# Optimization experiments

Hardware: AMD Instinct MI355X
Metric: run time of the kernel (lower is better)

## Reference

```python
import jax, jax.numpy as jnp
import numpy as np

H = 8            # heads actually used for the q/k/v split (256 = 8 * 32)
D = 32           # per-head dim
SCALE = 64 ** -0.5  # original code scales by init-arg dim_head**-0.5 (=64), not the actual split dim


def setup_inputs() -> dict:
    key = jax.random.key(0)
    ks = jax.random.split(key, 7)
    b, nq, nk, dim = 4, 2048, 2048, 256
    s = 1.0 / np.sqrt(dim).astype(np.float32)
    c2 = jax.random.normal(ks[0], (b, nk, dim), jnp.float32)
    c1 = jax.random.normal(ks[1], (b, nq, dim), jnp.float32)
    # weights stored as [in, out] so y = x @ W (equivalent to torch Linear)
    Wq = jax.random.normal(ks[2], (dim, dim), jnp.float32) * s
    Wk = jax.random.normal(ks[3], (dim, dim), jnp.float32) * s
    Wv = jax.random.normal(ks[4], (dim, dim), jnp.float32) * s
    Wo = jax.random.normal(ks[5], (dim, dim), jnp.float32) * s
    bo = jax.random.normal(ks[6], (dim,), jnp.float32) * 0.01
    return {"c2": c2, "c1": c1, "Wq": Wq, "Wk": Wk, "Wv": Wv, "Wo": Wo, "bo": bo}


def reference(c2, c1, Wq, Wk, Wv, Wo, bo):
    b, nq, dim = c1.shape
    nk = c2.shape[1]
    q = (c1 @ Wq).reshape(b, nq, H, D)   # queries from c1
    k = (c2 @ Wk).reshape(b, nk, H, D)   # keys from c2
    v = (c2 @ Wv).reshape(b, nk, H, D)   # values from c2
    dots = jnp.einsum('bqhd,bkhd->bhqk', q, k) * SCALE  # [b,H,nq,nk]
    attn = jax.nn.softmax(dots, axis=-1)
    out = jnp.einsum('bhqk,bkhd->bqhd', attn, v).reshape(b, nq, dim)
    return out @ Wo + bo  # to_out projection (dropout=0.0 -> identity)
```

## Files before the change

### kernel.cpp

```cpp
#include <hip/hip_runtime.h>
#include <hip/hip_bf16.h>

typedef __bf16 bf16;
typedef __bf16 bf16x4 __attribute__((ext_vector_type(4)));
typedef __bf16 bf16x8 __attribute__((ext_vector_type(8)));
typedef float f32x4 __attribute__((ext_vector_type(4)));

#define MFMA(a, b, c) __builtin_amdgcn_mfma_f32_16x16x32_bf16(a, b, c, 0, 0, 0)

#define QSCALE (0.125f * 1.44269504088896340736f)

#define OFF_Q  262144
#define OFF_K  (OFF_Q + 2097152)
#define OFF_VT (OFF_K + 2097152)
#define OFF_P  (OFF_VT + 2097152)
#define OFF_L  (OFF_P + 4194304)

static __device__ __forceinline__ float fexp2(float x) {
    return __builtin_amdgcn_exp2f(x);
}

#define GLL16(g, l)                                                              \
    __builtin_amdgcn_global_load_lds(                                            \
        (const __attribute__((address_space(1))) void*)(g),                      \
        (__attribute__((address_space(3))) void*)(l), 16, 0, 0)

__global__ __launch_bounds__(256) void k_wt(const float* __restrict__ Wq,
                                            const float* __restrict__ Wk,
                                            const float* __restrict__ Wv,
                                            const float* __restrict__ Wo,
                                            bf16* __restrict__ wts) {
    __shared__ __align__(16) bf16 tile[64][64];
    int rb = blockIdx.x, ob = blockIdx.y, mat = blockIdx.z;
    const float* src = (mat == 0) ? Wq : (mat == 1) ? Wk : (mat == 2) ? Wv : Wo;
    int t = threadIdx.x;
    int lr = t >> 4, lc = (t & 15) * 4;
#pragma unroll
    for (int rr = 0; rr < 4; ++rr) {
        int i = rb * 64 + rr * 16 + lr;
        f32x4 a = *reinterpret_cast<const f32x4*>(src + (size_t)i * 256 + ob * 64 + lc);
        bf16x4 v;
#pragma unroll
        for (int j = 0; j < 4; ++j) v[j] = (bf16)a[j];
        *reinterpret_cast<bf16x4*>(&tile[rr * 16 + lr][lc]) = v;
    }
    __syncthreads();
    int ol = t >> 2, ib = (t & 3) * 16;
    int o = ob * 64 + ol;
    bf16x8 v0, v1;
#pragma unroll
    for (int k = 0; k < 8; ++k) {
        v0[k] = tile[ib + k][ol];
        v1[k] = tile[ib + 8 + k][ol];
    }
    bf16* dst = wts + (size_t)mat * 65536 + (size_t)o * 256 + rb * 64 + ib;
    *reinterpret_cast<bf16x8*>(dst) = v0;
    *reinterpret_cast<bf16x8*>(dst + 8) = v1;
}

__global__ __launch_bounds__(384) void k_proj(const float* __restrict__ c1,
                                              const float* __restrict__ c2,
                                              const bf16* __restrict__ wts,
                                              bf16* __restrict__ qkv) {
    __shared__ __align__(16) bf16 sA[2][4096];
    int m = blockIdx.x;
    int t = threadIdx.x;

    if (t < 256) {
        int row = t >> 4, c0t = t & 15;
        const float* ap = c1 + ((size_t)m * 16 + row) * 256 + c0t * 16;
        f32x4 a0 = *reinterpret_cast<const f32x4*>(ap);
        f32x4 a1 = *reinterpret_cast<const f32x4*>(ap + 4);
        f32x4 a2 = *reinterpret_cast<const f32x4*>(ap + 8);
        f32x4 a3 = *reinterpret_cast<const f32x4*>(ap + 12);
        bf16x8 w0, w1;
#pragma unroll
        for (int j = 0; j < 4; ++j) {
            w0[j] = (bf16)a0[j]; w0[j + 4] = (bf16)a1[j];
            w1[j] = (bf16)a2[j]; w1[j + 4] = (bf16)a3[j];
        }
        int kc = c0t >> 1, gA = (c0t & 1) * 2;
        *reinterpret_cast<bf16x8*>(&sA[0][kc * 512 + (gA * 16 + row) * 8]) = w0;
        *reinterpret_cast<bf16x8*>(&sA[0][kc * 512 + ((gA + 1) * 16 + row) * 8]) = w1;
    }
    if (t >= 128) {
        int t2 = t - 128;
        int row = t2 >> 4, c0t = t2 & 15;
        const float* ap = c2 + ((size_t)m * 16 + row) * 256 + c0t * 16;
        f32x4 a0 = *reinterpret_cast<const f32x4*>(ap);
        f32x4 a1 = *reinterpret_cast<const f32x4*>(ap + 4);
        f32x4 a2 = *reinterpret_cast<const f32x4*>(ap + 8);
        f32x4 a3 = *reinterpret_cast<const f32x4*>(ap + 12);
        bf16x8 w0, w1;
#pragma unroll
        for (int j = 0; j < 4; ++j) {
            w0[j] = (bf16)a0[j]; w0[j + 4] = (bf16)a1[j];
            w1[j] = (bf16)a2[j]; w1[j + 4] = (bf16)a3[j];
        }
        int kc = c0t >> 1, gA = (c0t & 1) * 2;
        *reinterpret_cast<bf16x8*>(&sA[1][kc * 512 + (gA * 16 + row) * 8]) = w0;
        *reinterpret_cast<bf16x8*>(&sA[1][kc * 512 + ((gA + 1) * 16 + row) * 8]) = w1;
    }
    __syncthreads();

    int u = t >> 6;
    int lane = t & 63, cc = lane & 15, g = lane >> 4;
    int mat = u >> 1, nh = u & 1;
    const bf16* wt = wts + (size_t)mat * 65536;
    const bf16* sAp = sA[mat == 0 ? 0 : 1];

    f32x4 acc[8] = {};
#pragma unroll
    for (int kc = 0; kc < 8; ++kc) {
        bf16x8 af = *reinterpret_cast<const bf16x8*>(&sAp[kc * 512 + lane * 8]);
#pragma unroll
        for (int ct = 0; ct < 8; ++ct) {
            bf16x8 bf = *reinterpret_cast<const bf16x8*>(
                wt + (size_t)(nh * 128 + ct * 16 + cc) * 256 + kc * 32 + g * 8);
            acc[ct] = (mat == 2) ? MFMA(bf, af, acc[ct])
                                 : MFMA(af, bf, acc[ct]);
        }
    }

    if (mat != 2) {
        float os = (mat == 0) ? QSCALE : 1.0f;
        bf16* dst = qkv + (size_t)mat * 2097152;
#pragma unroll
        for (int ct = 0; ct < 8; ++ct) {
            int col = nh * 128 + ct * 16 + cc;
#pragma unroll
            for (int j = 0; j < 4; ++j)
                dst[(size_t)(m * 16 + 4 * g + j) * 256 + col] = (bf16)(acc[ct][j] * os);
        }
    } else {
        bf16* vt = qkv + (size_t)2 * 2097152;
        int b = (m * 16) >> 11, n0 = (m * 16) & 2047;
#pragma unroll
        for (int ct = 0; ct < 8; ++ct) {
#pragma unroll
            for (int j = 0; j < 4; ++j)
                vt[((size_t)b * 256 + nh * 128 + ct * 16 + 4 * g + j) * 2048 + n0 + cc] =
                    (bf16)acc[ct][j];
        }
    }
}

__global__ __launch_bounds__(256, 4) void k_attn(const bf16* __restrict__ Q,
                                                 const bf16* __restrict__ K,
                                                 const bf16* __restrict__ Vt,
                                                 bf16* __restrict__ P,
                                                 float* __restrict__ Lf) {
    __shared__ __align__(16) bf16 sK[4][2048];
    __shared__ __align__(16) bf16 sV[4][2048];

    int flat = blockIdx.x;
    int xcd = flat & 7;
    int sub = flat >> 3;
    int bh = xcd * 4 + (sub & 3);
    int rest = sub >> 2;
    int xtile = rest & 15;
    int split = rest >> 4;

    int b = bh >> 3, hd = bh & 7;
    int kv0 = split << 10;
    int lane = threadIdx.x & 63;
    int w = threadIdx.x >> 6;
    int cc = lane & 15, g = lane >> 4;
    int qrow0 = xtile * 128 + w * 32;

    const bf16* Qh = Q + (size_t)(b * 2048) * 256 + hd * 32;
    const bf16* Vth = Vt + (size_t)bh * 65536;
    size_t kbase0 = (size_t)(b * 2048) * 256 + hd * 32;

    bf16x8 qf[2];
#pragma unroll
    for (int h = 0; h < 2; ++h)
        qf[h] = *reinterpret_cast<const bf16x8*>(
            Qh + (size_t)(qrow0 + h * 16 + cc) * 256 + g * 8);

    int kp0 = 8 * (cc >> 2) + (cc & 3);
    int kperm[4];
#pragma unroll
    for (int r = 0; r < 4; ++r) kperm[r] = 32 * (r >> 1) + 4 * (r & 1) + kp0;

    int krow = w * 16 + (lane >> 2);
    int kcol = (lane & 3) * 8;
    int dv = w * 8 + (lane >> 3);
    int vcol = ((lane & 7) ^ (lane >> 3)) * 8;

    float lsum[2] = {0.f, 0.f};
    f32x4 oA[2] = {}, oB[2] = {};

#define STAGE(t, buf)                                                           \
    do {                                                                        \
        int kb_ = kv0 + (t) * 64;                                               \
        const bf16* kg_ = K + kbase0 + (size_t)(kb_ + krow) * 256 + kcol;       \
        GLL16(kg_, &sK[buf][w * 512]);                                          \
        const bf16* vg_ = Vth + (size_t)dv * 2048 + kb_ + vcol;                 \
        GLL16(vg_, &sV[buf][w * 512]);                                          \
    } while (0)

    STAGE(0, 0);
    STAGE(1, 1);

    for (int kt = 0; kt < 16; ++kt) {
        int cur = kt & 3;
        if (kt + 2 < 16) STAGE(kt + 2, (kt + 2) & 3);

        asm volatile("s_waitcnt vmcnt(4)" ::: "memory");
        __builtin_amdgcn_s_barrier();
        __builtin_amdgcn_sched_barrier(0);

        bf16x8 kf[4], vf[4];
#pragma unroll
        for (int r = 0; r < 4; ++r)
            kf[r] = *reinterpret_cast<const bf16x8*>(&sK[cur][kperm[r] * 32 + g * 8]);
#pragma unroll
        for (int dt = 0; dt < 2; ++dt)
#pragma unroll
            for (int kk = 0; kk < 2; ++kk) {
                int colp = (kk * 4 + g) ^ (cc & 7);
                vf[dt * 2 + kk] = *reinterpret_cast<const bf16x8*>(
                    &sV[cur][(dt * 16 + cc) * 64 + colp * 8]);
            }

#pragma unroll
        for (int h = 0; h < 2; ++h) {
            f32x4 z = {};
            f32x4 s[4];
            __builtin_amdgcn_s_setprio(1);
#pragma unroll
            for (int r = 0; r < 4; ++r) s[r] = MFMA(kf[r], qf[h], z);
            __builtin_amdgcn_s_setprio(0);

#pragma unroll
            for (int r = 0; r < 4; ++r)
#pragma unroll
                for (int j = 0; j < 4; ++j) s[r][j] = fexp2(s[r][j]);
            float t0 = (s[0][0] + s[0][1]) + (s[0][2] + s[0][3]);
            float t1 = (s[1][0] + s[1][1]) + (s[1][2] + s[1][3]);
            float t2 = (s[2][0] + s[2][1]) + (s[2][2] + s[2][3]);
            float t3 = (s[3][0] + s[3][1]) + (s[3][2] + s[3][3]);
            lsum[h] += (t0 + t1) + (t2 + t3);

            bf16x8 pb[2];
#pragma unroll
            for (int kk = 0; kk < 2; ++kk)
#pragma unroll
                for (int e = 0; e < 8; ++e)
                    pb[kk][e] = (bf16)s[2 * kk + (e >> 2)][e & 3];

            __builtin_amdgcn_s_setprio(1);
            oA[h] = MFMA(vf[0], pb[0], oA[h]);
            oA[h] = MFMA(vf[1], pb[1], oA[h]);
            oB[h] = MFMA(vf[2], pb[0], oB[h]);
            oB[h] = MFMA(vf[3], pb[1], oB[h]);
            __builtin_amdgcn_s_setprio(0);
        }
    }
#undef STAGE

#pragma unroll
    for (int h = 0; h < 2; ++h) {
        lsum[h] += __shfl_xor(lsum[h], 16);
        lsum[h] += __shfl_xor(lsum[h], 32);

        bf16* Pp = P + (size_t)split * 2097152 +
                   ((size_t)b * 2048 + qrow0 + h * 16 + cc) * 256 + hd * 32;
        bf16x4 w0, w1;
#pragma unroll
        for (int j = 0; j < 4; ++j) {
            w0[j] = (bf16)oA[h][j];
            w1[j] = (bf16)oB[h][j];
        }
        *reinterpret_cast<bf16x4*>(Pp + 4 * g) = w0;
        *reinterpret_cast<bf16x4*>(Pp + 16 + 4 * g) = w1;
        if (g == 0)
            Lf[(size_t)split * 65536 + (size_t)bh * 2048 + qrow0 + h * 16 + cc] = lsum[h];
    }
}

__global__ __launch_bounds__(64) void k_out(const bf16* __restrict__ P,
                                            const float* __restrict__ Lf,
                                            const bf16* __restrict__ WoT,
                                            const float* __restrict__ bo,
                                            float* __restrict__ out) {
    int m = blockIdx.x, nb = blockIdx.y;
    int l = threadIdx.x;
    int cc = l & 15, g = l >> 4;
    int arow = m * 16 + cc;
    int b = arow >> 11, n = arow & 2047;

    f32x4 acc[4] = {};
#pragma unroll
    for (int kc = 0; kc < 8; ++kc) {
        float l0 = Lf[(size_t)(b * 8 + kc) * 2048 + n];
        float l1 = Lf[65536 + (size_t)(b * 8 + kc) * 2048 + n];
        float inv = 1.0f / (l0 + l1);
        bf16x8 p0 = *reinterpret_cast<const bf16x8*>(
            P + (size_t)arow * 256 + kc * 32 + g * 8);
        bf16x8 p1 = *reinterpret_cast<const bf16x8*>(
            P + 2097152 + (size_t)arow * 256 + kc * 32 + g * 8);
        bf16x8 af;
#pragma unroll
        for (int e = 0; e < 8; ++e)
            af[e] = (bf16)(((float)p0[e] + (float)p1[e]) * inv);
#pragma unroll
        for (int ct = 0; ct < 4; ++ct) {
            bf16x8 bf = *reinterpret_cast<const bf16x8*>(
                WoT + (size_t)(nb * 64 + ct * 16 + cc) * 256 + kc * 32 + g * 8);
            acc[ct] = MFMA(af, bf, acc[ct]);
        }
    }
#pragma unroll
    for (int ct = 0; ct < 4; ++ct) {
        int col = nb * 64 + ct * 16 + cc;
        float bias = bo[col];
#pragma unroll
        for (int j = 0; j < 4; ++j) {
            int row = m * 16 + 4 * g + j;
            out[(size_t)row * 256 + col] = acc[ct][j] + bias;
        }
    }
}

extern "C" void kernel_launch(void* const* d_in, const int* in_sizes, int n_in,
                              void* d_out, int out_size, void* d_ws, size_t ws_size,
                              hipStream_t stream) {
    const float* c2 = (const float*)d_in[0];
    const float* c1 = (const float*)d_in[1];
    const float* Wq = (const float*)d_in[2];
    const float* Wk = (const float*)d_in[3];
    const float* Wv = (const float*)d_in[4];
    const float* Wo = (const float*)d_in[5];
    const float* bo = (const float*)d_in[6];
    float* out = (float*)d_out;

    bf16* ws = (bf16*)d_ws;
    bf16* wts = ws;
    bf16* Q = ws + OFF_Q;
    bf16* Vt = ws + OFF_VT;
    bf16* P = ws + OFF_P;
    float* Lf = (float*)(ws + OFF_L);

    k_wt<<<dim3(4, 4, 4), 256, 0, stream>>>(Wq, Wk, Wv, Wo, wts);
    k_proj<<<dim3(512), 384, 0, stream>>>(c1, c2, wts, Q);
    k_attn<<<dim3(1024), 256, 0, stream>>>(Q, ws + OFF_K, Vt, P, Lf);
    k_out<<<dim3(512, 4), 64, 0, stream>>>(P, Lf, wts + 3 * 65536, bo, out);
}
```

Baseline: 81.24 us.

## Double-buffer 128-key tiles with XOR-swizzled LDS and batch out-projection waves

The attention kernel now stages 128-key tiles into two LDS buffers, where it previously prefetched 64-key tiles two ahead into four buffers. Each staged tile is consumed in two halves, with a full __syncthreads per tile instead of a waitcnt plus barrier per 64 keys. K rows are stored with an XOR swizzle to avoid LDS bank conflicts, and the setprio hints are removed. The output projection now packs four 64-thread waves per block instead of one wave per block. The aim is fewer barriers and conflict-free LDS reads, at the cost of a shallower prefetch depth that may expose more load latency.

```diff
diff --git a/kernel.cpp b/kernel.cpp
--- a/kernel.cpp
+++ b/kernel.cpp
@@ -150,8 +150,8 @@
                                                  const bf16* __restrict__ Vt,
                                                  bf16* __restrict__ P,
                                                  float* __restrict__ Lf) {
-    __shared__ __align__(16) bf16 sK[4][2048];
-    __shared__ __align__(16) bf16 sV[4][2048];
+    __shared__ __align__(16) bf16 sK[2][4096];
+    __shared__ __align__(16) bf16 sV[2][4096];
 
     int flat = blockIdx.x;
     int xcd = flat & 7;
@@ -179,84 +179,93 @@
             Qh + (size_t)(qrow0 + h * 16 + cc) * 256 + g * 8);
 
     int kp0 = 8 * (cc >> 2) + (cc & 3);
-    int kperm[4];
-#pragma unroll
-    for (int r = 0; r < 4; ++r) kperm[r] = 32 * (r >> 1) + 4 * (r & 1) + kp0;
-
-    int krow = w * 16 + (lane >> 2);
-    int kcol = (lane & 3) * 8;
-    int dv = w * 8 + (lane >> 3);
-    int vcol = ((lane & 7) ^ (lane >> 3)) * 8;
+    int koff[4];
+#pragma unroll
+    for (int r = 0; r < 4; ++r) {
+        int kp = 32 * (r >> 1) + 4 * (r & 1) + kp0;
+        int fr = ((kp >> 1) ^ (kp >> 3)) & 3;
+        koff[r] = kp * 32 + ((g ^ fr) * 8);
+    }
+
+    int krowA = w * 32 + (lane >> 2);
+    int krowB = krowA + 16;
+    int fA = ((krowA >> 1) ^ (krowA >> 3)) & 3;
+    int fB = ((krowB >> 1) ^ (krowB >> 3)) & 3;
+    int kcolA = ((lane & 3) ^ fA) * 8;
+    int kcolB = ((lane & 3) ^ fB) * 8;
+    int dvA = w * 8 + (lane >> 4);
+    int dvB = dvA + 4;
+    int vcolA = ((lane & 15) ^ (dvA & 7)) * 8;
+    int vcolB = ((lane & 15) ^ (dvB & 7)) * 8;
 
     float lsum[2] = {0.f, 0.f};
     f32x4 oA[2] = {}, oB[2] = {};
 
 #define STAGE(t, buf)                                                           \
     do {                                                                        \
-        int kb_ = kv0 + (t) * 64;                                               \
-        const bf16* kg_ = K + kbase0 + (size_t)(kb_ + krow) * 256 + kcol;       \
-        GLL16(kg_, &sK[buf][w * 512]);                                          \
-        const bf16* vg_ = Vth + (size_t)dv * 2048 + kb_ + vcol;                 \
-        GLL16(vg_, &sV[buf][w * 512]);                                          \
+        int kb_ = kv0 + (t) * 128;                                              \
+        GLL16(K + kbase0 + (size_t)(kb_ + krowA) * 256 + kcolA,                 \
+              &sK[buf][w * 1024]);                                              \
+        GLL16(K + kbase0 + (size_t)(kb_ + krowB) * 256 + kcolB,                 \
+              &sK[buf][w * 1024 + 512]);                                        \
+        GLL16(Vth + (size_t)dvA * 2048 + kb_ + vcolA, &sV[buf][w * 1024]);      \
+        GLL16(Vth + (size_t)dvB * 2048 + kb_ + vcolB, &sV[buf][w * 1024 + 512]);\
     } while (0)
 
     STAGE(0, 0);
-    STAGE(1, 1);
-
-    for (int kt = 0; kt < 16; ++kt) {
-        int cur = kt & 3;
-        if (kt + 2 < 16) STAGE(kt + 2, (kt + 2) & 3);
-
-        asm volatile("s_waitcnt vmcnt(4)" ::: "memory");
-        __builtin_amdgcn_s_barrier();
-        __builtin_amdgcn_sched_barrier(0);
-
-        bf16x8 kf[4], vf[4];
-#pragma unroll
-        for (int r = 0; r < 4; ++r)
-            kf[r] = *reinterpret_cast<const bf16x8*>(&sK[cur][kperm[r] * 32 + g * 8]);
-#pragma unroll
-        for (int dt = 0; dt < 2; ++dt)
-#pragma unroll
-            for (int kk = 0; kk < 2; ++kk) {
-                int colp = (kk * 4 + g) ^ (cc & 7);
-                vf[dt * 2 + kk] = *reinterpret_cast<const bf16x8*>(
-                    &sV[cur][(dt * 16 + cc) * 64 + colp * 8]);
+    __syncthreads();
+
+    for (int t = 0; t < 8; ++t) {
+        int cur = t & 1;
+        if (t + 1 < 8) STAGE(t + 1, cur ^ 1);
+
+#pragma unroll
+        for (int half = 0; half < 2; ++half) {
+            bf16x8 kf[4], vf[4];
+#pragma unroll
+            for (int r = 0; r < 4; ++r)
+                kf[r] = *reinterpret_cast<const bf16x8*>(
+                    &sK[cur][half * 2048 + koff[r]]);
+#pragma unroll
+            for (int dt = 0; dt < 2; ++dt)
+#pragma unroll
+                for (int kk = 0; kk < 2; ++kk) {
+                    int chunk = half * 8 + ((kk * 4 + g) ^ (cc & 7));
+                    vf[dt * 2 + kk] = *reinterpret_cast<const bf16x8*>(
+                        &sV[cur][(dt * 16 + cc) * 128 + chunk * 8]);
+                }
+
+#pragma unroll
+            for (int h = 0; h < 2; ++h) {
+                f32x4 z = {};
+                f32x4 s[4];
+#pragma unroll
+                for (int r = 0; r < 4; ++r) s[r] = MFMA(kf[r], qf[h], z);
+
+#pragma unroll
+                for (int r = 0; r < 4; ++r)
+#pragma unroll
+                    for (int j = 0; j < 4; ++j) s[r][j] = fexp2(s[r][j]);
+                float t0 = (s[0][0] + s[0][1]) + (s[0][2] + s[0][3]);
+                float t1 = (s[1][0] + s[1][1]) + (s[1][2] + s[1][3]);
+                float t2 = (s[2][0] + s[2][1]) + (s[2][2] + s[2][3]);
+                float t3 = (s[3][0] + s[3][1]) + (s[3][2] + s[3][3]);
+                lsum[h] += (t0 + t1) + (t2 + t3);
+
+                bf16x8 pb[2];
+#pragma unroll
+                for (int kk = 0; kk < 2; ++kk)
+#pragma unroll
+                    for (int e = 0; e < 8; ++e)
+                        pb[kk][e] = (bf16)s[2 * kk + (e >> 2)][e & 3];
+
+                oA[h] = MFMA(vf[0], pb[0], oA[h]);
+                oA[h] = MFMA(vf[1], pb[1], oA[h]);
+                oB[h] = MFMA(vf[2], pb[0], oB[h]);
+                oB[h] = MFMA(vf[3], pb[1], oB[h]);
             }
-
-#pragma unroll
-        for (int h = 0; h < 2; ++h) {
-            f32x4 z = {};
-            f32x4 s[4];
-            __builtin_amdgcn_s_setprio(1);
-#pragma unroll
-            for (int r = 0; r < 4; ++r) s[r] = MFMA(kf[r], qf[h], z);
-            __builtin_amdgcn_s_setprio(0);
-
-#pragma unroll
-            for (int r = 0; r < 4; ++r)
-#pragma unroll
-                for (int j = 0; j < 4; ++j) s[r][j] = fexp2(s[r][j]);
-            float t0 = (s[0][0] + s[0][1]) + (s[0][2] + s[0][3]);
-            float t1 = (s[1][0] + s[1][1]) + (s[1][2] + s[1][3]);
-            float t2 = (s[2][0] + s[2][1]) + (s[2][2] + s[2][3]);
-            float t3 = (s[3][0] + s[3][1]) + (s[3][2] + s[3][3]);
-            lsum[h] += (t0 + t1) + (t2 + t3);
-
-            bf16x8 pb[2];
-#pragma unroll
-            for (int kk = 0; kk < 2; ++kk)
-#pragma unroll
-                for (int e = 0; e < 8; ++e)
-                    pb[kk][e] = (bf16)s[2 * kk + (e >> 2)][e & 3];
-
-            __builtin_amdgcn_s_setprio(1);
-            oA[h] = MFMA(vf[0], pb[0], oA[h]);
-            oA[h] = MFMA(vf[1], pb[1], oA[h]);
-            oB[h] = MFMA(vf[2], pb[0], oB[h]);
-            oB[h] = MFMA(vf[3], pb[1], oB[h]);
-            __builtin_amdgcn_s_setprio(0);
-        }
+        }
+        __syncthreads();
     }
 #undef STAGE
 
@@ -280,13 +289,13 @@
     }
 }
 
-__global__ __launch_bounds__(64) void k_out(const bf16* __restrict__ P,
-                                            const float* __restrict__ Lf,
-                                            const bf16* __restrict__ WoT,
-                                            const float* __restrict__ bo,
-                                            float* __restrict__ out) {
-    int m = blockIdx.x, nb = blockIdx.y;
-    int l = threadIdx.x;
+__global__ __launch_bounds__(256) void k_out(const bf16* __restrict__ P,
+                                             const float* __restrict__ Lf,
+                                             const bf16* __restrict__ WoT,
+                                             const float* __restrict__ bo,
+                                             float* __restrict__ out) {
+    int m = blockIdx.x * 4 + (threadIdx.x >> 6), nb = blockIdx.y;
+    int l = threadIdx.x & 63;
     int cc = l & 15, g = l >> 4;
     int arow = m * 16 + cc;
     int b = arow >> 11, n = arow & 2047;
@@ -346,5 +355,5 @@
     k_wt<<<dim3(4, 4, 4), 256, 0, stream>>>(Wq, Wk, Wv, Wo, wts);
     k_proj<<<dim3(512), 384, 0, stream>>>(c1, c2, wts, Q);
     k_attn<<<dim3(1024), 256, 0, stream>>>(Q, ws + OFF_K, Vt, P, Lf);
-    k_out<<<dim3(512, 4), 64, 0, stream>>>(P, Lf, wts + 3 * 65536, bo, out);
-}
+    k_out<<<dim3(128, 4), 256, 0, stream>>>(P, Lf, wts + 3 * 65536, bo, out);
+}
```

Measured after the change: 84.84 us. +4.4%, slower.
